# Kernel tuning notes

Measured on AMD Instinct MI355X. Metric: run time of the kernel, lower is better.

## Reference

```python
import jax, jax.numpy as jnp
import numpy as np

NUM_HEADS = 16


def setup_inputs() -> dict:
    key = jax.random.key(0)
    k1, k2, k3, k4 = jax.random.split(key, 4)
    in_dim, out_dim = 1024, 1024
    x = jax.random.normal(k1, (4, 2048, in_dim), dtype=jnp.float32)
    # nn.Linear weights stored as [out, in]; we keep that convention.
    s = 1.0 / np.sqrt(in_dim)
    Wq = jax.random.uniform(k2, (out_dim, in_dim), jnp.float32, -s, s)
    Wk = jax.random.uniform(k3, (out_dim, in_dim), jnp.float32, -s, s)
    Wv = jax.random.uniform(k4, (out_dim, in_dim), jnp.float32, -s, s)
    return {"x": x, "Wq": Wq, "Wk": Wk, "Wv": Wv}


def reference(x, Wq, Wk, Wv):
    b, n, _ = x.shape
    out_dim = Wq.shape[0]
    h = NUM_HEADS
    d = out_dim // h  # head_dim

    def split_heads(t):  # [b,n,out] -> [b,h,n,d]
        return t.reshape(b, n, h, d).transpose(0, 2, 1, 3)

    q = split_heads(x @ Wq.T)
    k = split_heads(x @ Wk.T)
    v = split_heads(x @ Wv.T)

    scores = jnp.einsum("bhqd,bhkd->bhqk", q, k) / jnp.sqrt(jnp.float32(d))
    causal = jnp.tril(jnp.ones((n, n), dtype=bool))
    scores = jnp.where(causal, scores, -jnp.inf)
    attn = jax.nn.softmax(scores, axis=-1)
    out = jnp.einsum("bhqk,bhkd->bhqd", attn, v)
    return out.transpose(0, 2, 1, 3).reshape(b, n, out_dim)
```

## Files before the change

kernel.cpp:

```cpp
#include <hip/hip_runtime.h>

typedef __attribute__((ext_vector_type(8))) short short8;
typedef __attribute__((ext_vector_type(4))) short short4v;
typedef __attribute__((ext_vector_type(4))) float floatx4;

#define GLOBAL_AS __attribute__((address_space(1)))
#define LDS_AS __attribute__((address_space(3)))

__device__ __forceinline__ short f2bs(float f) {
    union { float f; unsigned u; } v; v.f = f;
    unsigned r = v.u + 0x7fffu + ((v.u >> 16) & 1u);
    return (short)(r >> 16);
}

__device__ __forceinline__ short f2bs_fast(float f) {
    union { float f; unsigned u; } v; v.f = f;
    return (short)((v.u + 0x8000u) >> 16);
}

__global__ __launch_bounds__(256) void cast_f32_bf16(const float* __restrict__ in,
                                                     short* __restrict__ out, int n) {
    int i = (blockIdx.x * 256 + threadIdx.x) * 4;
    if (i < n) {
        float4 v = *(const float4*)(in + i);
        short4v o;
        o.x = f2bs(v.x); o.y = f2bs(v.y); o.z = f2bs(v.z); o.w = f2bs(v.w);
        *(short4v*)(out + i) = o;
    }
}

__global__ __launch_bounds__(256) void qkv_gemm(const short* __restrict__ xb,
                                                const short* __restrict__ wb,
                                                short* __restrict__ qout,
                                                short* __restrict__ kout,
                                                short* __restrict__ vtout) {
    __shared__ short As[128 * 32];
    __shared__ short Bs[128 * 32];
    const int K = 1024;
    int tid = threadIdx.x;
    int lane = tid & 63;
    int wid = tid >> 6;
    int quad = lane >> 4;
    int l16 = lane & 15;
    int wm = (wid >> 1) * 64;
    int wn = (wid & 1) * 64;
    int bm = blockIdx.x * 128;
    int bn = blockIdx.y * 128;
    const short* W = wb + (size_t)blockIdx.z * K * 1024;

    floatx4 acc[4][4];
#pragma unroll
    for (int i = 0; i < 4; i++)
#pragma unroll
        for (int j = 0; j < 4; j++) acc[i][j] = (floatx4){0.f, 0.f, 0.f, 0.f};

    int arow = tid >> 2;
    int achunk = ((tid & 3) ^ (arow & 3)) * 8;
    int asw = (quad ^ (l16 & 3)) * 8;

    for (int kk = 0; kk < K; kk += 32) {
        __syncthreads();
#pragma unroll
        for (int i = 0; i < 2; i++) {
            const short* g = xb + (size_t)(bm + i * 64 + arow) * K + kk + achunk;
            __builtin_amdgcn_global_load_lds((const GLOBAL_AS void*)g,
                                             (LDS_AS void*)(As + i * 2048 + tid * 8), 16, 0, 0);
        }
#pragma unroll
        for (int i = 0; i < 2; i++) {
            const short* g = W + (size_t)(bn + i * 64 + arow) * K + kk + achunk;
            __builtin_amdgcn_global_load_lds((const GLOBAL_AS void*)g,
                                             (LDS_AS void*)(Bs + i * 2048 + tid * 8), 16, 0, 0);
        }
        __syncthreads();

        short8 af[4], bf[4];
#pragma unroll
        for (int i = 0; i < 4; i++)
            af[i] = *(const short8*)(As + (wm + i * 16 + l16) * 32 + asw);
#pragma unroll
        for (int j = 0; j < 4; j++)
            bf[j] = *(const short8*)(Bs + (wn + j * 16 + l16) * 32 + asw);
#pragma unroll
        for (int i = 0; i < 4; i++)
#pragma unroll
            for (int j = 0; j < 4; j++)
                acc[i][j] = __builtin_amdgcn_mfma_f32_16x16x32_bf16(af[i], bf[j], acc[i][j], 0, 0, 0);
    }

    if (blockIdx.z == 2) {
#pragma unroll
        for (int i = 0; i < 4; i++) {
#pragma unroll
            for (int j = 0; j < 4; j++) {
                int m = bm + wm + i * 16 + quad * 4;
                int c = bn + wn + j * 16 + l16;
                int b = m >> 11, nn = m & 2047, h = c >> 6, dd = c & 63;
                short4v pk;
                pk.x = f2bs(acc[i][j][0]);
                pk.y = f2bs(acc[i][j][1]);
                pk.z = f2bs(acc[i][j][2]);
                pk.w = f2bs(acc[i][j][3]);
                *(short4v*)(vtout + ((size_t)(b * 16 + h) * 64 + dd) * 2048 + nn) = pk;
            }
        }
    } else {
        short* dst = (blockIdx.z == 0) ? qout : kout;
        float qs = (blockIdx.z == 0) ? 0.180336881f : 1.0f;
#pragma unroll
        for (int i = 0; i < 4; i++) {
#pragma unroll
            for (int j = 0; j < 4; j++) {
#pragma unroll
                for (int r = 0; r < 4; r++) {
                    int m = bm + wm + i * 16 + quad * 4 + r;
                    int c = bn + wn + j * 16 + l16;
                    dst[((size_t)((m >> 11) * 16 + (c >> 6)) * 2048 + (m & 2047)) * 64 + (c & 63)] =
                        f2bs(acc[i][j][r] * qs);
                }
            }
        }
    }
}

__global__ __launch_bounds__(512, 4) void attn(const short* __restrict__ q,
                                               const short* __restrict__ k,
                                               const short* __restrict__ vt,
                                               float* __restrict__ out) {
    __shared__ short Ks[64 * 64];
    __shared__ short Vs[64 * 64];
    __shared__ short Ps[8 * 16 * 72];

    int tid = threadIdx.x;
    int lane = tid & 63;
    int wid = tid >> 6;
    int quad = lane >> 4;
    int l16 = lane & 15;
    int b = blockIdx.z, h = blockIdx.y;

    const short* qp = q + (size_t)(b * 16 + h) * 2048 * 64;
    const short* kp = k + (size_t)(b * 16 + h) * 2048 * 64;
    const short* vp = vt + (size_t)(b * 16 + h) * 64 * 2048;

    int srow = tid >> 3;
    int schunk = ((tid & 7) ^ (srow & 7)) * 8;
    int ksw = l16 & 7;
    short* pw = Ps + wid * 16 * 72;

    for (int phase = 0; phase < 2; phase++) {
        int qt = (phase == 0) ? blockIdx.x : (15 - blockIdx.x);
        int qbase = qt * 128;
        int qrow_w = qbase + wid * 16;

        short8 qf0 = *(const short8*)(qp + (size_t)(qrow_w + l16) * 64 + quad * 8);
        short8 qf1 = *(const short8*)(qp + (size_t)(qrow_w + l16) * 64 + 32 + quad * 8);

        floatx4 oacc[4];
#pragma unroll
        for (int d = 0; d < 4; d++) oacc[d] = (floatx4){0.f, 0.f, 0.f, 0.f};
        float lrow[4] = {0.f, 0.f, 0.f, 0.f};

        int kv_end = qbase + 128;
        for (int kvb = 0; kvb < kv_end; kvb += 64) {
            __syncthreads();
            {
                const short* g = kp + (size_t)(kvb + srow) * 64 + schunk;
                __builtin_amdgcn_global_load_lds((const GLOBAL_AS void*)g,
                                                 (LDS_AS void*)(Ks + tid * 8), 16, 0, 0);
            }
            {
                const short* g = vp + (size_t)srow * 2048 + kvb + schunk;
                __builtin_amdgcn_global_load_lds((const GLOBAL_AS void*)g,
                                                 (LDS_AS void*)(Vs + tid * 8), 16, 0, 0);
            }
            __syncthreads();

            if (kvb <= qrow_w + 15) {
                floatx4 sacc[4];
#pragma unroll
                for (int j = 0; j < 4; j++) sacc[j] = (floatx4){0.f, 0.f, 0.f, 0.f};
#pragma unroll
                for (int s = 0; s < 2; s++) {
#pragma unroll
                    for (int j = 0; j < 4; j++) {
                        short8 kf = *(const short8*)(Ks + (j * 16 + l16) * 64 +
                                                     ((s * 4 + quad) ^ ksw) * 8);
                        sacc[j] = __builtin_amdgcn_mfma_f32_16x16x32_bf16(
                            (s == 0) ? qf0 : qf1, kf, sacc[j], 0, 0, 0);
                    }
                }

                bool interior = (kvb + 63 <= qrow_w);
#pragma unroll
                for (int r = 0; r < 4; r++) {
                    int qr = qrow_w + quad * 4 + r;
#pragma unroll
                    for (int j = 0; j < 4; j++) {
                        float p = __builtin_amdgcn_exp2f(sacc[j][r]);
                        if (!interior) p = (kvb + j * 16 + l16 > qr) ? 0.f : p;
                        sacc[j][r] = p;
                        lrow[r] += p;
                    }
                }

#pragma unroll
                for (int j = 0; j < 4; j++)
#pragma unroll
                    for (int r = 0; r < 4; r++)
                        pw[(quad * 4 + r) * 72 + j * 16 + l16] = f2bs_fast(sacc[j][r]);
                __threadfence_block();

#pragma unroll
                for (int s = 0; s < 2; s++) {
                    short8 pf = *(const short8*)(pw + l16 * 72 + s * 32 + quad * 8);
#pragma unroll
                    for (int d = 0; d < 4; d++) {
                        short8 vf = *(const short8*)(Vs + (d * 16 + l16) * 64 +
                                                     ((s * 4 + quad) ^ ksw) * 8);
                        oacc[d] = __builtin_amdgcn_mfma_f32_16x16x32_bf16(pf, vf, oacc[d], 0, 0, 0);
                    }
                }
            }
        }

#pragma unroll
        for (int r = 0; r < 4; r++) {
#pragma unroll
            for (int off = 1; off < 16; off <<= 1) lrow[r] += __shfl_xor(lrow[r], off);
        }
        float inv[4];
#pragma unroll
        for (int r = 0; r < 4; r++) inv[r] = 1.0f / lrow[r];

#pragma unroll
        for (int d = 0; d < 4; d++) {
#pragma unroll
            for (int r = 0; r < 4; r++) {
                int nn = qrow_w + quad * 4 + r;
                out[((size_t)b * 2048 + nn) * 1024 + h * 64 + d * 16 + l16] = oacc[d][r] * inv[r];
            }
        }
    }
}

extern "C" void kernel_launch(void* const* d_in, const int* in_sizes, int n_in,
                              void* d_out, int out_size, void* d_ws, size_t ws_size,
                              hipStream_t stream) {
    const float* x = (const float*)d_in[0];
    const float* Wq = (const float*)d_in[1];
    const float* Wk = (const float*)d_in[2];
    const float* Wv = (const float*)d_in[3];
    float* out = (float*)d_out;
    char* ws = (char*)d_ws;

    short* xb = (short*)ws;
    short* wb = (short*)(ws + (16u << 20));
    short* qb = (short*)(ws + (22u << 20));
    short* kb = (short*)(ws + (38u << 20));
    short* vtb = (short*)(ws + (54u << 20));

    cast_f32_bf16<<<8192, 256, 0, stream>>>(x, xb, 8192 * 1024);
    cast_f32_bf16<<<1024, 256, 0, stream>>>(Wq, wb, 1024 * 1024);
    cast_f32_bf16<<<1024, 256, 0, stream>>>(Wk, wb + 1024 * 1024, 1024 * 1024);
    cast_f32_bf16<<<1024, 256, 0, stream>>>(Wv, wb + 2 * 1024 * 1024, 1024 * 1024);

    qkv_gemm<<<dim3(64, 8, 3), 256, 0, stream>>>(xb, wb, qb, kb, vtb);
    attn<<<dim3(8, 16, 4), 512, 0, stream>>>(qb, kb, vtb, out);
}
```

Measured before the change: 234.7 us.

## Merge cast kernels, widen GEMM K-tile, use 128-wide KV tiles with MFMA row sums

The four cast launches become one kernel that picks its source by block index. The QKV GEMM now stages 64-wide K slices per sync, with an 8-way XOR swizzle, which halves barrier count. The attention kernel processes 128 keys per iteration instead of 64, and computes the softmax denominator with an MFMA against a vector of ones instead of per-thread sums plus shuffles. These cut launch and synchronisation overhead. The cost is more LDS per block, which can lower occupancy, plus extra masked work on the wider diagonal tiles.

```diff
diff --git a/kernel.cpp b/kernel.cpp
--- a/kernel.cpp
+++ b/kernel.cpp
@@ -18,15 +18,30 @@
     return (short)((v.u + 0x8000u) >> 16);
 }
 
-__global__ __launch_bounds__(256) void cast_f32_bf16(const float* __restrict__ in,
-                                                     short* __restrict__ out, int n) {
-    int i = (blockIdx.x * 256 + threadIdx.x) * 4;
-    if (i < n) {
-        float4 v = *(const float4*)(in + i);
-        short4v o;
-        o.x = f2bs(v.x); o.y = f2bs(v.y); o.z = f2bs(v.z); o.w = f2bs(v.w);
-        *(short4v*)(out + i) = o;
-    }
+__global__ __launch_bounds__(256) void cast_all(const float* __restrict__ x,
+                                                const float* __restrict__ Wq,
+                                                const float* __restrict__ Wk,
+                                                const float* __restrict__ Wv,
+                                                short* __restrict__ xb,
+                                                short* __restrict__ wb) {
+    int b = blockIdx.x;
+    int t = threadIdx.x;
+    const float* src;
+    short* dst;
+    int idx;
+    if (b < 8192) {
+        src = x; dst = xb; idx = b * 1024 + t * 4;
+    } else {
+        int r = b - 8192;
+        int wz = r >> 10;
+        src = (wz == 0) ? Wq : (wz == 1) ? Wk : Wv;
+        dst = wb + wz * (1 << 20);
+        idx = (r & 1023) * 1024 + t * 4;
+    }
+    float4 v = *(const float4*)(src + idx);
+    short4v o;
+    o.x = f2bs(v.x); o.y = f2bs(v.y); o.z = f2bs(v.z); o.w = f2bs(v.w);
+    *(short4v*)(dst + idx) = o;
 }
 
 __global__ __launch_bounds__(256) void qkv_gemm(const short* __restrict__ xb,
@@ -34,8 +49,8 @@
                                                 short* __restrict__ qout,
                                                 short* __restrict__ kout,
                                                 short* __restrict__ vtout) {
-    __shared__ short As[128 * 32];
-    __shared__ short Bs[128 * 32];
+    __shared__ short As[128 * 64];
+    __shared__ short Bs[128 * 64];
     const int K = 1024;
     int tid = threadIdx.x;
     int lane = tid & 63;
@@ -54,38 +69,41 @@
 #pragma unroll
         for (int j = 0; j < 4; j++) acc[i][j] = (floatx4){0.f, 0.f, 0.f, 0.f};
 
-    int arow = tid >> 2;
-    int achunk = ((tid & 3) ^ (arow & 3)) * 8;
-    int asw = (quad ^ (l16 & 3)) * 8;
-
-    for (int kk = 0; kk < K; kk += 32) {
+    int srow = tid >> 3;
+    int ssw = ((tid & 7) ^ (srow & 7)) * 8;
+
+    for (int kk = 0; kk < K; kk += 64) {
         __syncthreads();
 #pragma unroll
-        for (int i = 0; i < 2; i++) {
-            const short* g = xb + (size_t)(bm + i * 64 + arow) * K + kk + achunk;
+        for (int l = 0; l < 4; l++) {
+            const short* g = xb + (size_t)(bm + srow + l * 32) * K + kk + ssw;
             __builtin_amdgcn_global_load_lds((const GLOBAL_AS void*)g,
-                                             (LDS_AS void*)(As + i * 2048 + tid * 8), 16, 0, 0);
-        }
-#pragma unroll
-        for (int i = 0; i < 2; i++) {
-            const short* g = W + (size_t)(bn + i * 64 + arow) * K + kk + achunk;
+                                             (LDS_AS void*)(As + tid * 8 + l * 2048), 16, 0, 0);
+        }
+#pragma unroll
+        for (int l = 0; l < 4; l++) {
+            const short* g = W + (size_t)(bn + srow + l * 32) * K + kk + ssw;
             __builtin_amdgcn_global_load_lds((const GLOBAL_AS void*)g,
-                                             (LDS_AS void*)(Bs + i * 2048 + tid * 8), 16, 0, 0);
+                                             (LDS_AS void*)(Bs + tid * 8 + l * 2048), 16, 0, 0);
         }
         __syncthreads();
 
-        short8 af[4], bf[4];
-#pragma unroll
-        for (int i = 0; i < 4; i++)
-            af[i] = *(const short8*)(As + (wm + i * 16 + l16) * 32 + asw);
-#pragma unroll
-        for (int j = 0; j < 4; j++)
-            bf[j] = *(const short8*)(Bs + (wn + j * 16 + l16) * 32 + asw);
-#pragma unroll
-        for (int i = 0; i < 4; i++)
+#pragma unroll
+        for (int s = 0; s < 2; s++) {
+            int slot = ((s * 4 + quad) ^ (l16 & 7)) * 8;
+            short8 af[4], bf[4];
+#pragma unroll
+            for (int i = 0; i < 4; i++)
+                af[i] = *(const short8*)(As + (wm + i * 16 + l16) * 64 + slot);
 #pragma unroll
             for (int j = 0; j < 4; j++)
-                acc[i][j] = __builtin_amdgcn_mfma_f32_16x16x32_bf16(af[i], bf[j], acc[i][j], 0, 0, 0);
+                bf[j] = *(const short8*)(Bs + (wn + j * 16 + l16) * 64 + slot);
+#pragma unroll
+            for (int i = 0; i < 4; i++)
+#pragma unroll
+                for (int j = 0; j < 4; j++)
+                    acc[i][j] = __builtin_amdgcn_mfma_f32_16x16x32_bf16(af[i], bf[j], acc[i][j], 0, 0, 0);
+        }
     }
 
     if (blockIdx.z == 2) {
@@ -127,9 +145,9 @@
                                                const short* __restrict__ k,
                                                const short* __restrict__ vt,
                                                float* __restrict__ out) {
-    __shared__ short Ks[64 * 64];
-    __shared__ short Vs[64 * 64];
-    __shared__ short Ps[8 * 16 * 72];
+    __shared__ short Ks[128 * 64];
+    __shared__ short Vs[64 * 128];
+    __shared__ short Ps[8 * 16 * 136];
 
     int tid = threadIdx.x;
     int lane = tid & 63;
@@ -142,10 +160,17 @@
     const short* kp = k + (size_t)(b * 16 + h) * 2048 * 64;
     const short* vp = vt + (size_t)(b * 16 + h) * 64 * 2048;
 
-    int srow = tid >> 3;
-    int schunk = ((tid & 7) ^ (srow & 7)) * 8;
-    int ksw = l16 & 7;
-    short* pw = Ps + wid * 16 * 72;
+    int krow = tid >> 3;
+    int ksw = ((tid & 7) ^ (krow & 7)) * 8;
+    int vd = tid >> 4;
+    int vc = tid & 15;
+    int vsw = ((vc & 8) | ((vc ^ vd) & 7)) * 8;
+
+    short* pw = Ps + wid * (16 * 136);
+
+    short8 ones;
+#pragma unroll
+    for (int i = 0; i < 8; i++) ones[i] = (short)0x3F80;
 
     for (int phase = 0; phase < 2; phase++) {
         int qt = (phase == 0) ? blockIdx.x : (15 - blockIdx.x);
@@ -158,79 +183,70 @@
         floatx4 oacc[4];
 #pragma unroll
         for (int d = 0; d < 4; d++) oacc[d] = (floatx4){0.f, 0.f, 0.f, 0.f};
-        float lrow[4] = {0.f, 0.f, 0.f, 0.f};
-
-        int kv_end = qbase + 128;
-        for (int kvb = 0; kvb < kv_end; kvb += 64) {
+        floatx4 lacc = (floatx4){0.f, 0.f, 0.f, 0.f};
+
+        for (int kvb = 0; kvb <= qbase; kvb += 128) {
             __syncthreads();
-            {
-                const short* g = kp + (size_t)(kvb + srow) * 64 + schunk;
+#pragma unroll
+            for (int l = 0; l < 2; l++) {
+                const short* g = kp + (size_t)(kvb + krow + l * 64) * 64 + ksw;
                 __builtin_amdgcn_global_load_lds((const GLOBAL_AS void*)g,
-                                                 (LDS_AS void*)(Ks + tid * 8), 16, 0, 0);
-            }
-            {
-                const short* g = vp + (size_t)srow * 2048 + kvb + schunk;
+                                                 (LDS_AS void*)(Ks + tid * 8 + l * 4096), 16, 0, 0);
+            }
+#pragma unroll
+            for (int l = 0; l < 2; l++) {
+                const short* g = vp + (size_t)(vd + l * 32) * 2048 + kvb + vsw;
                 __builtin_amdgcn_global_load_lds((const GLOBAL_AS void*)g,
-                                                 (LDS_AS void*)(Vs + tid * 8), 16, 0, 0);
+                                                 (LDS_AS void*)(Vs + tid * 8 + l * 4096), 16, 0, 0);
             }
             __syncthreads();
 
-            if (kvb <= qrow_w + 15) {
-                floatx4 sacc[4];
-#pragma unroll
-                for (int j = 0; j < 4; j++) sacc[j] = (floatx4){0.f, 0.f, 0.f, 0.f};
-#pragma unroll
-                for (int s = 0; s < 2; s++) {
-#pragma unroll
-                    for (int j = 0; j < 4; j++) {
-                        short8 kf = *(const short8*)(Ks + (j * 16 + l16) * 64 +
-                                                     ((s * 4 + quad) ^ ksw) * 8);
-                        sacc[j] = __builtin_amdgcn_mfma_f32_16x16x32_bf16(
-                            (s == 0) ? qf0 : qf1, kf, sacc[j], 0, 0, 0);
-                    }
-                }
-
-                bool interior = (kvb + 63 <= qrow_w);
-#pragma unroll
-                for (int r = 0; r < 4; r++) {
-                    int qr = qrow_w + quad * 4 + r;
-#pragma unroll
-                    for (int j = 0; j < 4; j++) {
-                        float p = __builtin_amdgcn_exp2f(sacc[j][r]);
-                        if (!interior) p = (kvb + j * 16 + l16 > qr) ? 0.f : p;
-                        sacc[j][r] = p;
-                        lrow[r] += p;
-                    }
-                }
-
-#pragma unroll
-                for (int j = 0; j < 4; j++)
-#pragma unroll
-                    for (int r = 0; r < 4; r++)
-                        pw[(quad * 4 + r) * 72 + j * 16 + l16] = f2bs_fast(sacc[j][r]);
-                __threadfence_block();
-
-#pragma unroll
-                for (int s = 0; s < 2; s++) {
-                    short8 pf = *(const short8*)(pw + l16 * 72 + s * 32 + quad * 8);
-#pragma unroll
-                    for (int d = 0; d < 4; d++) {
-                        short8 vf = *(const short8*)(Vs + (d * 16 + l16) * 64 +
-                                                     ((s * 4 + quad) ^ ksw) * 8);
-                        oacc[d] = __builtin_amdgcn_mfma_f32_16x16x32_bf16(pf, vf, oacc[d], 0, 0, 0);
-                    }
-                }
-            }
-        }
-
-#pragma unroll
-        for (int r = 0; r < 4; r++) {
-#pragma unroll
-            for (int off = 1; off < 16; off <<= 1) lrow[r] += __shfl_xor(lrow[r], off);
-        }
+            floatx4 sacc[8];
+#pragma unroll
+            for (int j = 0; j < 8; j++) sacc[j] = (floatx4){0.f, 0.f, 0.f, 0.f};
+#pragma unroll
+            for (int s = 0; s < 2; s++) {
+#pragma unroll
+                for (int j = 0; j < 8; j++) {
+                    int row = j * 16 + l16;
+                    short8 kf = *(const short8*)(Ks + row * 64 +
+                                                 (((s * 4 + quad) ^ (row & 7)) * 8));
+                    sacc[j] = __builtin_amdgcn_mfma_f32_16x16x32_bf16(
+                        (s == 0) ? qf0 : qf1, kf, sacc[j], 0, 0, 0);
+                }
+            }
+
+            bool diag = (kvb + 127 > qrow_w);
+#pragma unroll
+            for (int r = 0; r < 4; r++) {
+                int qr = qrow_w + quad * 4 + r;
+#pragma unroll
+                for (int j = 0; j < 8; j++) {
+                    float p = __builtin_amdgcn_exp2f(sacc[j][r]);
+                    if (diag) p = (kvb + j * 16 + l16 > qr) ? 0.f : p;
+                    pw[(quad * 4 + r) * 136 + j * 16 + l16] = f2bs_fast(p);
+                }
+            }
+            __threadfence_block();
+
+#pragma unroll
+            for (int s = 0; s < 4; s++) {
+                short8 pf = *(const short8*)(pw + l16 * 136 + s * 32 + quad * 8);
+                lacc = __builtin_amdgcn_mfma_f32_16x16x32_bf16(pf, ones, lacc, 0, 0, 0);
+#pragma unroll
+                for (int d = 0; d < 4; d++) {
+                    int row = d * 16 + l16;
+                    int c = s * 4 + quad;
+                    int slot = (c & 8) | ((c ^ (row & 7)) & 7);
+                    short8 vf = *(const short8*)(Vs + row * 128 + slot * 8);
+                    oacc[d] = __builtin_amdgcn_mfma_f32_16x16x32_bf16(pf, vf, oacc[d], 0, 0, 0);
+                }
+            }
+        }
+
         float inv[4];
 #pragma unroll
-        for (int r = 0; r < 4; r++) inv[r] = 1.0f / lrow[r];
+        for (int r = 0; r < 4; r++) inv[r] = 1.0f / lacc[r];
 
 #pragma unroll
         for (int d = 0; d < 4; d++) {
@@ -259,11 +275,7 @@
     short* kb = (short*)(ws + (38u << 20));
     short* vtb = (short*)(ws + (54u << 20));
 
-    cast_f32_bf16<<<8192, 256, 0, stream>>>(x, xb, 8192 * 1024);
-    cast_f32_bf16<<<1024, 256, 0, stream>>>(Wq, wb, 1024 * 1024);
-    cast_f32_bf16<<<1024, 256, 0, stream>>>(Wk, wb + 1024 * 1024, 1024 * 1024);
-    cast_f32_bf16<<<1024, 256, 0, stream>>>(Wv, wb + 2 * 1024 * 1024, 1024 * 1024);
-
+    cast_all<<<8192 + 3 * 1024, 256, 0, stream>>>(x, Wq, Wk, Wv, xb, wb);
     qkv_gemm<<<dim3(64, 8, 3), 256, 0, stream>>>(xb, wb, qb, kb, vtb);
     attn<<<dim3(8, 16, 4), 512, 0, stream>>>(qb, kb, vtb, out);
 }
```

New measurement: 225.5 us. 3.9% less time.
